# Performance work log

Measured on AMD Instinct MI355X. Metric: run time of the kernel, lower is better.

The kernel has to match this reference:

```python
import jax, jax.numpy as jnp
import numpy as np

N_NODES = 100000
N_EDGES = 640000
D_IN = 128
D_H = 128


def setup_inputs() -> dict:
    key = jax.random.key(0)
    ks = jax.random.split(key, 24)
    def W(k, shp):
        return jax.random.normal(k, shp, dtype=jnp.float32) * 0.05
    inp = {
        "x": jax.random.normal(ks[0], (N_NODES, D_IN), dtype=jnp.float32),
        "src": jax.random.randint(ks[1], (N_EDGES,), 0, N_NODES, dtype=jnp.int32),
        "dst": jax.random.randint(ks[2], (N_EDGES,), 0, N_NODES, dtype=jnp.int32),
        "neg_src": jax.random.randint(ks[3], (N_EDGES,), 0, N_NODES, dtype=jnp.int32),
        "neg_dst": jax.random.randint(ks[4], (N_EDGES,), 0, N_NODES, dtype=jnp.int32),
        # SAGEConv layer 1/2/3: fc_self weight, fc_neigh weight (stored [in,out]), bias
        "Ws1": W(ks[5], (D_IN, D_H)), "Wn1": W(ks[6], (D_IN, D_H)), "b1": jnp.zeros((D_H,), jnp.float32),
        "Ws2": W(ks[7], (D_H, D_H)), "Wn2": W(ks[8], (D_H, D_H)), "b2": jnp.zeros((D_H,), jnp.float32),
        "Ws3": W(ks[9], (D_H, D_H)), "Wn3": W(ks[10], (D_H, D_H)), "b3": jnp.zeros((D_H,), jnp.float32),
        # MLPPredictor: W1 [2h,h], W2 [h,1]
        "Wp1": W(ks[11], (2 * D_H, D_H)), "bp1": jnp.zeros((D_H,), jnp.float32),
        "Wp2": W(ks[12], (D_H, 1)), "bp2": jnp.zeros((1,), jnp.float32),
    }
    return inp


def _sage_mean(x, src, dst, Ws, Wn, b):
    # DGL SAGEConv 'mean': rst = fc_self(h) + fc_neigh(mean_{in-neighbors}(h)) + bias
    n = x.shape[0]
    msum = jax.ops.segment_sum(x[src], dst, num_segments=n)        # [N, d]
    deg = jax.ops.segment_sum(jnp.ones_like(src, dtype=x.dtype), dst, num_segments=n)
    mean = msum / jnp.clip(deg, 1.0)[:, None]                      # zero for isolated nodes
    return x @ Ws + mean @ Wn + b


def _edge_score(h, s, d, Wp1, bp1, Wp2, bp2):
    z = jnp.concatenate([h[s], h[d]], axis=1)                      # [E, 2h]
    return (jax.nn.relu(z @ Wp1 + bp1) @ Wp2 + bp2)[:, 0]          # [E]


def reference(x, src, dst, neg_src, neg_dst,
              Ws1, Wn1, b1, Ws2, Wn2, b2, Ws3, Wn3, b3,
              Wp1, bp1, Wp2, bp2):
    h = _sage_mean(x, src, dst, Ws1, Wn1, b1)
    h = _sage_mean(h, src, dst, Ws2, Wn2, b2)
    h = _sage_mean(h, src, dst, Ws3, Wn3, b3)
    pos = _edge_score(h, src, dst, Wp1, bp1, Wp2, bp2)
    neg = _edge_score(h, neg_src, neg_dst, Wp1, bp1, Wp2, bp2)
    return (pos, neg)
```

## Files before the change

kernel.cpp:

```cpp
#include <hip/hip_runtime.h>

#define N_NODES 100000
#define N_EDGES 640000
#define D 128
#define SCAN_TILE 1024
#define SCAN_BLOCKS ((N_NODES + SCAN_TILE - 1) / SCAN_TILE)

typedef __attribute__((ext_vector_type(8))) short bf16x8;
typedef __attribute__((ext_vector_type(4))) float f32x4;

__device__ __forceinline__ unsigned short f32_to_bf16(float f) {
  union { float f; unsigned int u; } v; v.f = f;
  unsigned int u = v.u;
  unsigned int r = (u + 0x7fffu + ((u >> 16) & 1u)) >> 16;
  return (unsigned short)r;
}
__device__ __forceinline__ float bf16_lo(unsigned int u) { return __uint_as_float(u << 16); }
__device__ __forceinline__ float bf16_hi(unsigned int u) { return __uint_as_float(u & 0xffff0000u); }

__device__ __forceinline__ void acc8(float* a, uint4 r) {
  a[0] += bf16_lo(r.x); a[1] += bf16_hi(r.x);
  a[2] += bf16_lo(r.y); a[3] += bf16_hi(r.y);
  a[4] += bf16_lo(r.z); a[5] += bf16_hi(r.z);
  a[6] += bf16_lo(r.w); a[7] += bf16_hi(r.w);
}

__global__ void zero_i32(int* __restrict__ p, int n) {
  int i = blockIdx.x * blockDim.x + threadIdx.x;
  if (i < n) p[i] = 0;
}

__global__ void f32_to_bf16_vec(const float* __restrict__ in, unsigned short* __restrict__ out, int n4) {
  int i = blockIdx.x * blockDim.x + threadIdx.x;
  if (i < n4) {
    float4 v = ((const float4*)in)[i];
    ushort4 o;
    o.x = f32_to_bf16(v.x); o.y = f32_to_bf16(v.y);
    o.z = f32_to_bf16(v.z); o.w = f32_to_bf16(v.w);
    ((ushort4*)out)[i] = o;
  }
}

__global__ void transpose_w(const float* __restrict__ W0, const float* __restrict__ W1,
                            const float* __restrict__ W2, const float* __restrict__ W3,
                            const float* __restrict__ W4, const float* __restrict__ W5,
                            const float* __restrict__ W6, const float* __restrict__ W7,
                            unsigned short* __restrict__ wt) {
  int id = blockIdx.x * 256 + threadIdx.x;
  int mat = id >> 14;
  int rem = id & 16383;
  int n = rem >> 7, k = rem & 127;
  const float* Wm = mat < 4 ? (mat < 2 ? (mat == 0 ? W0 : W1) : (mat == 2 ? W2 : W3))
                            : (mat < 6 ? (mat == 4 ? W4 : W5) : (mat == 6 ? W6 : W7));
  wt[id] = f32_to_bf16(Wm[k * D + n]);
}

__global__ void hist_kernel(const int* __restrict__ dst, int* __restrict__ deg, int E) {
  int i = blockIdx.x * blockDim.x + threadIdx.x;
  if (i < E) atomicAdd(&deg[dst[i]], 1);
}

__global__ void scan_blocksum(const int* __restrict__ deg, int* __restrict__ partial, int n) {
  __shared__ int lds[256];
  const int tid = threadIdx.x;
  const int base = blockIdx.x * SCAN_TILE + tid * 4;
  int s = 0;
#pragma unroll
  for (int j = 0; j < 4; ++j) {
    int i = base + j;
    if (i < n) s += deg[i];
  }
  lds[tid] = s;
  __syncthreads();
  for (int off = 128; off > 0; off >>= 1) {
    if (tid < off) lds[tid] += lds[tid + off];
    __syncthreads();
  }
  if (tid == 0) partial[blockIdx.x] = lds[0];
}

__global__ void scan_offsets(int* __restrict__ partial, int* __restrict__ row_start, int nb, int n) {
  __shared__ int lds[128];
  const int tid = threadIdx.x;
  int v = (tid < nb) ? partial[tid] : 0;
  lds[tid] = v;
  __syncthreads();
  for (int off = 1; off < 128; off <<= 1) {
    int t = (tid >= off) ? lds[tid - off] : 0;
    __syncthreads();
    lds[tid] += t;
    __syncthreads();
  }
  if (tid < nb) partial[tid] = (tid == 0) ? 0 : lds[tid - 1];
  if (tid == 0) row_start[n] = lds[nb - 1];
}

__global__ void scan_final(const int* __restrict__ deg, const int* __restrict__ partial,
                           int* __restrict__ row_start, int n) {
  __shared__ int lds[256];
  const int tid = threadIdx.x;
  const int base = blockIdx.x * SCAN_TILE + tid * 4;
  int d[4];
  int s = 0;
#pragma unroll
  for (int j = 0; j < 4; ++j) {
    int i = base + j;
    d[j] = (i < n) ? deg[i] : 0;
    s += d[j];
  }
  lds[tid] = s;
  __syncthreads();
  for (int off = 1; off < 256; off <<= 1) {
    int t = (tid >= off) ? lds[tid - off] : 0;
    __syncthreads();
    lds[tid] += t;
    __syncthreads();
  }
  int pre = partial[blockIdx.x] + lds[tid] - s;
#pragma unroll
  for (int j = 0; j < 4; ++j) {
    int i = base + j;
    if (i < n) {
      row_start[i] = pre;
      pre += d[j];
    }
  }
}

__global__ void fill_kernel(const int* __restrict__ src, const int* __restrict__ dst,
                            const int* __restrict__ row_start, int* __restrict__ cursor,
                            int* __restrict__ esrc, int E) {
  int i = blockIdx.x * blockDim.x + threadIdx.x;
  if (i < E) {
    int d = dst[i];
    int pos = atomicAdd(&cursor[d], 1);
    esrc[row_start[d] + pos] = src[i];
  }
}

template <bool PRED>
__global__ __launch_bounds__(256) void layer_fused(
    const unsigned short* __restrict__ hin,
    const int* __restrict__ row_start, const int* __restrict__ esrc,
    const unsigned short* __restrict__ Wts, const unsigned short* __restrict__ Wtn,
    const float* __restrict__ bias,
    const unsigned short* __restrict__ WtA, const unsigned short* __restrict__ WtB,
    const float* __restrict__ biasA,
    unsigned short* __restrict__ out0, unsigned short* __restrict__ out1, int M) {
  __shared__ unsigned short wl[64][136];
  __shared__ unsigned short mt[64][136];
  const int tid = threadIdx.x;
  const int lane = tid & 63;
  const int wave = tid >> 6;
  const int m0 = blockIdx.x * 64;
  const int row = lane & 15;
  const int q = lane >> 4;
  const int mw = m0 + wave * 16;
  const int mload = min(mw + row, M - 1);

  auto stage64 = [&](const unsigned short* W, int half) {
#pragma unroll
    for (int i = 0; i < 4; ++i) {
      int seg = i * 256 + tid;
      int r = seg >> 4, o = (seg & 15) * 8;
      *reinterpret_cast<bf16x8*>(&wl[r][o]) =
          *reinterpret_cast<const bf16x8*>(W + (size_t)(half * 64 + r) * D + o);
    }
  };
  auto mfma_half = [&](bf16x8* a, f32x4* accp) {
#pragma unroll
    for (int s = 0; s < 4; ++s)
#pragma unroll
      for (int t = 0; t < 4; ++t) {
        bf16x8 b = *reinterpret_cast<const bf16x8*>(&wl[t * 16 + row][s * 32 + q * 8]);
        accp[t] = __builtin_amdgcn_mfma_f32_16x16x32_bf16(a[s], b, accp[t], 0, 0, 0);
      }
  };
  auto epilogue = [&](f32x4* accp, const float* bvec, unsigned short* dst) {
#pragma unroll
    for (int t = 0; t < 8; ++t) {
      const int col = t * 16 + row;
      const float bv = bvec ? bvec[col] : 0.f;
#pragma unroll
      for (int r = 0; r < 4; ++r)
        mt[wave * 16 + q * 4 + r][col] = f32_to_bf16(accp[t][r] + bv);
    }
    __syncthreads();
#pragma unroll
    for (int i = 0; i < 4; ++i) {
      int idx = i * 256 + tid;
      int r2 = idx >> 4;
      int c8 = (idx & 15) * 8;
      int m = m0 + r2;
      if (m < M)
        *reinterpret_cast<uint4*>(dst + (size_t)m * D + c8) =
            *reinterpret_cast<const uint4*>(&mt[r2][c8]);
    }
  };

  bf16x8 ah[4];
#pragma unroll
  for (int s = 0; s < 4; ++s)
    ah[s] = *reinterpret_cast<const bf16x8*>(hin + (size_t)mload * D + s * 32 + q * 8);

  stage64(Wts, 0);

  {
    const int g = tid >> 4;
    const int fl = tid & 15;
    for (int j = 0; j < 4; ++j) {
      const int node = m0 + g * 4 + j;
      float ac[8] = {0.f, 0.f, 0.f, 0.f, 0.f, 0.f, 0.f, 0.f};
      if (node < M) {
        const int s0 = row_start[node], s1 = row_start[node + 1];
        int e = s0;
        for (; e + 4 <= s1; e += 4) {
          int i0 = esrc[e], i1 = esrc[e + 1], i2 = esrc[e + 2], i3 = esrc[e + 3];
          uint4 r0 = *(const uint4*)(hin + (size_t)i0 * D + fl * 8);
          uint4 r1 = *(const uint4*)(hin + (size_t)i1 * D + fl * 8);
          uint4 r2 = *(const uint4*)(hin + (size_t)i2 * D + fl * 8);
          uint4 r3 = *(const uint4*)(hin + (size_t)i3 * D + fl * 8);
          acc8(ac, r0); acc8(ac, r1); acc8(ac, r2); acc8(ac, r3);
        }
        for (; e < s1; ++e) {
          uint4 r0 = *(const uint4*)(hin + (size_t)esrc[e] * D + fl * 8);
          acc8(ac, r0);
        }
        const float inv = 1.0f / (float)max(s1 - s0, 1);
#pragma unroll
        for (int k = 0; k < 8; ++k) ac[k] *= inv;
      }
      uint4 o;
      o.x = (unsigned)f32_to_bf16(ac[0]) | ((unsigned)f32_to_bf16(ac[1]) << 16);
      o.y = (unsigned)f32_to_bf16(ac[2]) | ((unsigned)f32_to_bf16(ac[3]) << 16);
      o.z = (unsigned)f32_to_bf16(ac[4]) | ((unsigned)f32_to_bf16(ac[5]) << 16);
      o.w = (unsigned)f32_to_bf16(ac[6]) | ((unsigned)f32_to_bf16(ac[7]) << 16);
      *reinterpret_cast<uint4*>(&mt[g * 4 + j][fl * 8]) = o;
    }
  }
  __syncthreads();

  const int lrow = wave * 16 + row;
  bf16x8 am[4];
#pragma unroll
  for (int s = 0; s < 4; ++s)
    am[s] = *reinterpret_cast<const bf16x8*>(&mt[lrow][s * 32 + q * 8]);

  f32x4 acc[8];
#pragma unroll
  for (int t = 0; t < 8; ++t) acc[t] = (f32x4){0.f, 0.f, 0.f, 0.f};

  mfma_half(ah, acc);
  __syncthreads(); stage64(Wts, 1); __syncthreads();
  mfma_half(ah, acc + 4);
  __syncthreads(); stage64(Wtn, 0); __syncthreads();
  mfma_half(am, acc);
  __syncthreads(); stage64(Wtn, 1); __syncthreads();
  mfma_half(am, acc + 4);

  if (!PRED) {
    epilogue(acc, bias, out0);
    return;
  }

  __syncthreads();
#pragma unroll
  for (int t = 0; t < 8; ++t) {
    const int col = t * 16 + row;
    const float bv = bias[col];
#pragma unroll
    for (int r = 0; r < 4; ++r)
      mt[wave * 16 + q * 4 + r][col] = f32_to_bf16(acc[t][r] + bv);
  }
  stage64(WtA, 0);
  __syncthreads();
  bf16x8 ap[4];
#pragma unroll
  for (int s = 0; s < 4; ++s)
    ap[s] = *reinterpret_cast<const bf16x8*>(&mt[lrow][s * 32 + q * 8]);

#pragma unroll
  for (int t = 0; t < 8; ++t) acc[t] = (f32x4){0.f, 0.f, 0.f, 0.f};
  mfma_half(ap, acc);
  __syncthreads(); stage64(WtA, 1); __syncthreads();
  mfma_half(ap, acc + 4);
  epilogue(acc, biasA, out0);
  __syncthreads(); stage64(WtB, 0); __syncthreads();
#pragma unroll
  for (int t = 0; t < 8; ++t) acc[t] = (f32x4){0.f, 0.f, 0.f, 0.f};
  mfma_half(ap, acc);
  __syncthreads(); stage64(WtB, 1); __syncthreads();
  mfma_half(ap, acc + 4);
  epilogue(acc, nullptr, out1);
}

__device__ __forceinline__ float relu_dot8(uint4 a, uint4 b, float4 w0, float4 w1) {
  return fmaxf(bf16_lo(a.x) + bf16_lo(b.x), 0.f) * w0.x +
         fmaxf(bf16_hi(a.x) + bf16_hi(b.x), 0.f) * w0.y +
         fmaxf(bf16_lo(a.y) + bf16_lo(b.y), 0.f) * w0.z +
         fmaxf(bf16_hi(a.y) + bf16_hi(b.y), 0.f) * w0.w +
         fmaxf(bf16_lo(a.z) + bf16_lo(b.z), 0.f) * w1.x +
         fmaxf(bf16_hi(a.z) + bf16_hi(b.z), 0.f) * w1.y +
         fmaxf(bf16_lo(a.w) + bf16_lo(b.w), 0.f) * w1.z +
         fmaxf(bf16_hi(a.w) + bf16_hi(b.w), 0.f) * w1.w;
}

__global__ __launch_bounds__(256) void edge_score4(
    const unsigned short* __restrict__ A, const unsigned short* __restrict__ B,
    const int* __restrict__ ss, const int* __restrict__ dd,
    const float* __restrict__ Wp2, const float* __restrict__ bp2,
    float* __restrict__ out, int E) {
  const int t = blockIdx.x * blockDim.x + threadIdx.x;
  const int g = t >> 4;
  const int fl = t & 15;
  const int e0 = g * 4;
  if (e0 >= E) return;
  const int4 s4 = *(const int4*)(ss + e0);
  const int4 d4 = *(const int4*)(dd + e0);
  const float4 w0 = *(const float4*)(Wp2 + fl * 8);
  const float4 w1 = *(const float4*)(Wp2 + fl * 8 + 4);
  const size_t fo = (size_t)(fl * 8);

  uint4 a0 = *(const uint4*)(A + (((size_t)s4.x << 7) + fo));
  uint4 b0 = *(const uint4*)(B + (((size_t)d4.x << 7) + fo));
  uint4 a1 = *(const uint4*)(A + (((size_t)s4.y << 7) + fo));
  uint4 b1 = *(const uint4*)(B + (((size_t)d4.y << 7) + fo));
  uint4 a2 = *(const uint4*)(A + (((size_t)s4.z << 7) + fo));
  uint4 b2 = *(const uint4*)(B + (((size_t)d4.z << 7) + fo));
  uint4 a3 = *(const uint4*)(A + (((size_t)s4.w << 7) + fo));
  uint4 b3 = *(const uint4*)(B + (((size_t)d4.w << 7) + fo));

  float p0 = relu_dot8(a0, b0, w0, w1);
  float p1 = relu_dot8(a1, b1, w0, w1);
  float p2 = relu_dot8(a2, b2, w0, w1);
  float p3 = relu_dot8(a3, b3, w0, w1);

  p0 += __shfl_xor(p0, 1); p1 += __shfl_xor(p1, 1); p2 += __shfl_xor(p2, 1); p3 += __shfl_xor(p3, 1);
  p0 += __shfl_xor(p0, 2); p1 += __shfl_xor(p1, 2); p2 += __shfl_xor(p2, 2); p3 += __shfl_xor(p3, 2);
  p0 += __shfl_xor(p0, 4); p1 += __shfl_xor(p1, 4); p2 += __shfl_xor(p2, 4); p3 += __shfl_xor(p3, 4);
  p0 += __shfl_xor(p0, 8); p1 += __shfl_xor(p1, 8); p2 += __shfl_xor(p2, 8); p3 += __shfl_xor(p3, 8);

  if (fl == 0) {
    const float bv = bp2[0];
    *reinterpret_cast<float4*>(out + e0) = make_float4(p0 + bv, p1 + bv, p2 + bv, p3 + bv);
  }
}

extern "C" void kernel_launch(void* const* d_in, const int* in_sizes, int n_in,
                              void* d_out, int out_size, void* d_ws, size_t ws_size,
                              hipStream_t stream) {
  const float* x = (const float*)d_in[0];
  const int* src = (const int*)d_in[1];
  const int* dst = (const int*)d_in[2];
  const int* nsrc = (const int*)d_in[3];
  const int* ndst = (const int*)d_in[4];
  const float* Ws1 = (const float*)d_in[5];
  const float* Wn1 = (const float*)d_in[6];
  const float* b1 = (const float*)d_in[7];
  const float* Ws2 = (const float*)d_in[8];
  const float* Wn2 = (const float*)d_in[9];
  const float* b2 = (const float*)d_in[10];
  const float* Ws3 = (const float*)d_in[11];
  const float* Wn3 = (const float*)d_in[12];
  const float* b3 = (const float*)d_in[13];
  const float* Wp1 = (const float*)d_in[14];
  const float* bp1 = (const float*)d_in[15];
  const float* Wp2 = (const float*)d_in[16];
  const float* bp2 = (const float*)d_in[17];
  float* out = (float*)d_out;

  char* ws = (char*)d_ws;
  size_t off = 0;
  auto alloc = [&](size_t bytes) -> void* {
    void* p = ws + off;
    off += (bytes + 255) & ~(size_t)255;
    return p;
  };
  const size_t NODE_F32 = sizeof(float) * (size_t)N_NODES * D;
  char* region0 = (char*)alloc(NODE_F32);
  char* region1 = (char*)alloc(NODE_F32);
  int* row_start = (int*)alloc(sizeof(int) * (N_NODES + 1));
  int* deg = (int*)alloc(sizeof(int) * N_NODES * 2);
  int* cursor = deg + N_NODES;
  int* esrc = (int*)alloc(sizeof(int) * N_EDGES);
  int* partial = (int*)alloc(sizeof(int) * 128);
  unsigned short* wt = (unsigned short*)alloc(sizeof(unsigned short) * 8 * D * D);
  (void)ws_size;

  unsigned short* xb = (unsigned short*)region0;
  unsigned short* hA = (unsigned short*)region1;
  unsigned short* hB = hA + (size_t)N_NODES * D;
  unsigned short* Ab = xb;
  unsigned short* Bb = xb + (size_t)N_NODES * D;

  f32_to_bf16_vec<<<(N_NODES * D / 4 + 255) / 256, 256, 0, stream>>>(x, xb, N_NODES * D / 4);
  transpose_w<<<512, 256, 0, stream>>>(Ws1, Wn1, Ws2, Wn2, Ws3, Wn3, Wp1, Wp1 + D * D, wt);

  zero_i32<<<(2 * N_NODES + 255) / 256, 256, 0, stream>>>(deg, 2 * N_NODES);
  hist_kernel<<<(N_EDGES + 255) / 256, 256, 0, stream>>>(dst, deg, N_EDGES);
  scan_blocksum<<<SCAN_BLOCKS, 256, 0, stream>>>(deg, partial, N_NODES);
  scan_offsets<<<1, 128, 0, stream>>>(partial, row_start, SCAN_BLOCKS, N_NODES);
  scan_final<<<SCAN_BLOCKS, 256, 0, stream>>>(deg, partial, row_start, N_NODES);
  fill_kernel<<<(N_EDGES + 255) / 256, 256, 0, stream>>>(src, dst, row_start, cursor, esrc, N_EDGES);

  const int layerBlocks = (N_NODES + 63) / 64;
  const int edgeBlocks = (N_EDGES / 4 * 16) / 256;

  layer_fused<false><<<layerBlocks, 256, 0, stream>>>(
      xb, row_start, esrc, wt, wt + 16384, b1, nullptr, nullptr, nullptr, hA, nullptr, N_NODES);
  layer_fused<false><<<layerBlocks, 256, 0, stream>>>(
      hA, row_start, esrc, wt + 2 * 16384, wt + 3 * 16384, b2, nullptr, nullptr, nullptr, hB, nullptr, N_NODES);
  layer_fused<true><<<layerBlocks, 256, 0, stream>>>(
      hB, row_start, esrc, wt + 4 * 16384, wt + 5 * 16384, b3, wt + 6 * 16384, wt + 7 * 16384, bp1,
      Ab, Bb, N_NODES);
  edge_score4<<<edgeBlocks, 256, 0, stream>>>(Ab, Bb, src, dst, Wp2, bp2, out, N_EDGES);
  edge_score4<<<edgeBlocks, 256, 0, stream>>>(Ab, Bb, nsrc, ndst, Wp2, bp2, out + N_EDGES, N_EDGES);
}
```

Baseline: 481.6 us.

## Split fused SAGE layer into separate gather-mean and MLP kernels

Each SAGE layer's neighbour mean aggregation moves out of the fused MFMA kernel into its own kernel, with one node per 16 threads writing a bf16 mean buffer to global memory. The MLP kernel then loads both the self features and the mean rows straight from global memory. The aim is more parallelism and better latency hiding for the irregular gather, which before ran only 64 nodes per block, four nodes per thread serially. In exchange each layer pays an extra write and read of a 25.6 MB mean buffer plus three more kernel launches.

```diff
diff --git a/kernel.cpp b/kernel.cpp
--- a/kernel.cpp
+++ b/kernel.cpp
@@ -138,10 +138,44 @@
   }
 }
 
-template <bool PRED>
-__global__ __launch_bounds__(256) void layer_fused(
+__global__ __launch_bounds__(256) void gather_mean(
     const unsigned short* __restrict__ hin,
     const int* __restrict__ row_start, const int* __restrict__ esrc,
+    unsigned short* __restrict__ mean, int M) {
+  const int t = blockIdx.x * blockDim.x + threadIdx.x;
+  const int node = t >> 4;
+  const int fl = t & 15;
+  if (node >= M) return;
+  const int s0 = row_start[node], s1 = row_start[node + 1];
+  float ac[8] = {0.f, 0.f, 0.f, 0.f, 0.f, 0.f, 0.f, 0.f};
+  int e = s0;
+  for (; e + 4 <= s1; e += 4) {
+    int i0 = esrc[e], i1 = esrc[e + 1], i2 = esrc[e + 2], i3 = esrc[e + 3];
+    uint4 r0 = *(const uint4*)(hin + (((size_t)i0) << 7) + fl * 8);
+    uint4 r1 = *(const uint4*)(hin + (((size_t)i1) << 7) + fl * 8);
+    uint4 r2 = *(const uint4*)(hin + (((size_t)i2) << 7) + fl * 8);
+    uint4 r3 = *(const uint4*)(hin + (((size_t)i3) << 7) + fl * 8);
+    acc8(ac, r0); acc8(ac, r1); acc8(ac, r2); acc8(ac, r3);
+  }
+  for (; e < s1; ++e) {
+    uint4 r0 = *(const uint4*)(hin + (((size_t)esrc[e]) << 7) + fl * 8);
+    acc8(ac, r0);
+  }
+  const float inv = 1.0f / (float)max(s1 - s0, 1);
+#pragma unroll
+  for (int k = 0; k < 8; ++k) ac[k] *= inv;
+  uint4 o;
+  o.x = (unsigned)f32_to_bf16(ac[0]) | ((unsigned)f32_to_bf16(ac[1]) << 16);
+  o.y = (unsigned)f32_to_bf16(ac[2]) | ((unsigned)f32_to_bf16(ac[3]) << 16);
+  o.z = (unsigned)f32_to_bf16(ac[4]) | ((unsigned)f32_to_bf16(ac[5]) << 16);
+  o.w = (unsigned)f32_to_bf16(ac[6]) | ((unsigned)f32_to_bf16(ac[7]) << 16);
+  *reinterpret_cast<uint4*>(mean + (((size_t)node) << 7) + fl * 8) = o;
+}
+
+template <bool PRED>
+__global__ __launch_bounds__(256) void layer_mlp(
+    const unsigned short* __restrict__ hin,
+    const unsigned short* __restrict__ mean,
     const unsigned short* __restrict__ Wts, const unsigned short* __restrict__ Wtn,
     const float* __restrict__ bias,
     const unsigned short* __restrict__ WtA, const unsigned short* __restrict__ WtB,
@@ -157,6 +191,7 @@
   const int q = lane >> 4;
   const int mw = m0 + wave * 16;
   const int mload = min(mw + row, M - 1);
+  const int lrow = wave * 16 + row;
 
   auto stage64 = [&](const unsigned short* W, int half) {
 #pragma unroll
@@ -198,53 +233,14 @@
     }
   };
 
-  bf16x8 ah[4];
-#pragma unroll
-  for (int s = 0; s < 4; ++s)
+  stage64(Wts, 0);
+  bf16x8 ah[4], am[4];
+#pragma unroll
+  for (int s = 0; s < 4; ++s) {
     ah[s] = *reinterpret_cast<const bf16x8*>(hin + (size_t)mload * D + s * 32 + q * 8);
-
-  stage64(Wts, 0);
-
-  {
-    const int g = tid >> 4;
-    const int fl = tid & 15;
-    for (int j = 0; j < 4; ++j) {
-      const int node = m0 + g * 4 + j;
-      float ac[8] = {0.f, 0.f, 0.f, 0.f, 0.f, 0.f, 0.f, 0.f};
-      if (node < M) {
-        const int s0 = row_start[node], s1 = row_start[node + 1];
-        int e = s0;
-        for (; e + 4 <= s1; e += 4) {
-          int i0 = esrc[e], i1 = esrc[e + 1], i2 = esrc[e + 2], i3 = esrc[e + 3];
-          uint4 r0 = *(const uint4*)(hin + (size_t)i0 * D + fl * 8);
-          uint4 r1 = *(const uint4*)(hin + (size_t)i1 * D + fl * 8);
-          uint4 r2 = *(const uint4*)(hin + (size_t)i2 * D + fl * 8);
-          uint4 r3 = *(const uint4*)(hin + (size_t)i3 * D + fl * 8);
-          acc8(ac, r0); acc8(ac, r1); acc8(ac, r2); acc8(ac, r3);
-        }
-        for (; e < s1; ++e) {
-          uint4 r0 = *(const uint4*)(hin + (size_t)esrc[e] * D + fl * 8);
-          acc8(ac, r0);
-        }
-        const float inv = 1.0f / (float)max(s1 - s0, 1);
-#pragma unroll
-        for (int k = 0; k < 8; ++k) ac[k] *= inv;
-      }
-      uint4 o;
-      o.x = (unsigned)f32_to_bf16(ac[0]) | ((unsigned)f32_to_bf16(ac[1]) << 16);
-      o.y = (unsigned)f32_to_bf16(ac[2]) | ((unsigned)f32_to_bf16(ac[3]) << 16);
-      o.z = (unsigned)f32_to_bf16(ac[4]) | ((unsigned)f32_to_bf16(ac[5]) << 16);
-      o.w = (unsigned)f32_to_bf16(ac[6]) | ((unsigned)f32_to_bf16(ac[7]) << 16);
-      *reinterpret_cast<uint4*>(&mt[g * 4 + j][fl * 8]) = o;
-    }
-  }
-  __syncthreads();
-
-  const int lrow = wave * 16 + row;
-  bf16x8 am[4];
-#pragma unroll
-  for (int s = 0; s < 4; ++s)
-    am[s] = *reinterpret_cast<const bf16x8*>(&mt[lrow][s * 32 + q * 8]);
+    am[s] = *reinterpret_cast<const bf16x8*>(mean + (size_t)mload * D + s * 32 + q * 8);
+  }
+  __syncthreads();
 
   f32x4 acc[8];
 #pragma unroll
@@ -379,6 +375,7 @@
   const size_t NODE_F32 = sizeof(float) * (size_t)N_NODES * D;
   char* region0 = (char*)alloc(NODE_F32);
   char* region1 = (char*)alloc(NODE_F32);
+  unsigned short* meanb = (unsigned short*)alloc(sizeof(unsigned short) * (size_t)N_NODES * D);
   int* row_start = (int*)alloc(sizeof(int) * (N_NODES + 1));
   int* deg = (int*)alloc(sizeof(int) * N_NODES * 2);
   int* cursor = deg + N_NODES;
@@ -403,15 +400,19 @@
   scan_final<<<SCAN_BLOCKS, 256, 0, stream>>>(deg, partial, row_start, N_NODES);
   fill_kernel<<<(N_EDGES + 255) / 256, 256, 0, stream>>>(src, dst, row_start, cursor, esrc, N_EDGES);
 
-  const int layerBlocks = (N_NODES + 63) / 64;
+  const int gatherBlocks = (N_NODES * 16 + 255) / 256;
+  const int mlpBlocks = (N_NODES + 63) / 64;
   const int edgeBlocks = (N_EDGES / 4 * 16) / 256;
 
-  layer_fused<false><<<layerBlocks, 256, 0, stream>>>(
-      xb, row_start, esrc, wt, wt + 16384, b1, nullptr, nullptr, nullptr, hA, nullptr, N_NODES);
-  layer_fused<false><<<layerBlocks, 256, 0, stream>>>(
-      hA, row_start, esrc, wt + 2 * 16384, wt + 3 * 16384, b2, nullptr, nullptr, nullptr, hB, nullptr, N_NODES);
-  layer_fused<true><<<layerBlocks, 256, 0, stream>>>(
-      hB, row_start, esrc, wt + 4 * 16384, wt + 5 * 16384, b3, wt + 6 * 16384, wt + 7 * 16384, bp1,
+  gather_mean<<<gatherBlocks, 256, 0, stream>>>(xb, row_start, esrc, meanb, N_NODES);
+  layer_mlp<false><<<mlpBlocks, 256, 0, stream>>>(
+      xb, meanb, wt, wt + 16384, b1, nullptr, nullptr, nullptr, hA, nullptr, N_NODES);
+  gather_mean<<<gatherBlocks, 256, 0, stream>>>(hA, row_start, esrc, meanb, N_NODES);
+  layer_mlp<false><<<mlpBlocks, 256, 0, stream>>>(
+      hA, meanb, wt + 2 * 16384, wt + 3 * 16384, b2, nullptr, nullptr, nullptr, hB, nullptr, N_NODES);
+  gather_mean<<<gatherBlocks, 256, 0, stream>>>(hB, row_start, esrc, meanb, N_NODES);
+  layer_mlp<true><<<mlpBlocks, 256, 0, stream>>>(
+      hB, meanb, wt + 4 * 16384, wt + 5 * 16384, b3, wt + 6 * 16384, wt + 7 * 16384, bp1,
       Ab, Bb, N_NODES);
   edge_score4<<<edgeBlocks, 256, 0, stream>>>(Ab, Bb, src, dst, Wp2, bp2, out, N_EDGES);
   edge_score4<<<edgeBlocks, 256, 0, stream>>>(Ab, Bb, nsrc, ndst, Wp2, bp2, out + N_EDGES, N_EDGES);
```

Result: faster. 457.0 us (-5.1%).
